# Optimization experiments

Measured on AMD Instinct MI355X. Metric: run time of the kernel, lower is better.

## Reference

```python
import jax, jax.numpy as jnp
import numpy as np

B, C_IN, N, T, E, C_OUT = 128, 32, 325, 24, 3, 64


def setup_inputs() -> dict:
    key = jax.random.key(0)
    kx, ka, kw, kb = jax.random.split(key, 4)
    x = jax.random.normal(kx, (B, C_IN, N, T), dtype=jnp.float32)
    supports = jax.random.normal(ka, (E, N, N), dtype=jnp.float32) * (1.0 / np.sqrt(N))
    # 1x1 Conv2d params: weight [c_out, c_in*(edge_dim+1)], bias [c_out]
    fan_in = C_IN * (E + 1)
    W = jax.random.normal(kw, (C_OUT, fan_in), dtype=jnp.float32) * (1.0 / np.sqrt(fan_in))
    b = jax.random.normal(kb, (C_OUT,), dtype=jnp.float32) * 0.05
    return {"x": x, "supports": supports, "W": W, "b": b}


def reference(x, supports, W, b):
    # x: [B, C, N, T], supports: [E, N, N]
    Bb, C, Nn, Tt = x.shape
    # nconv for every support at once: einsum 'bcvt,vw->bcwt' batched over E
    diff = jnp.einsum('bcvt,evw->becwt', x, supports)  # [B, E, C, N, T]
    # concat [x] + diffused copies along channel dim -> [B, (E+1)*C, N, T]
    h = jnp.concatenate([x[:, None], diff], axis=1).reshape(Bb, -1, Nn, Tt)
    # 1x1 conv == channel-mixing matmul; squeeze(-1) is a no-op since T > 1
    out = jnp.einsum('bkvt,ok->bovt', h, W) + b[None, :, None, None]
    return out  # [B, c_out, N, T]
```

## Files before the change

### kernel.cpp

```cpp
#include <hip/hip_runtime.h>
#include <hip/hip_bf16.h>

typedef short bf16x8 __attribute__((ext_vector_type(8)));
typedef short bf16x4 __attribute__((ext_vector_type(4)));
typedef float f32x4  __attribute__((ext_vector_type(4)));

static constexpr int Bb   = 128;
static constexpr int Cin  = 32;
static constexpr int Nn   = 325;
static constexpr int Tt   = 24;
static constexpr int Cout = 64;
static constexpr int NKS  = 11;
static constexpr int WP   = 336;
static constexpr int NWT  = 21;
static constexpr size_t XTB_ELEMS = (size_t)Bb * NKS * (Tt * Cin) * 32;
static constexpr size_t STP_ELEMS = (size_t)4 * NKS * WP * 32;
static constexpr size_t WB_ELEMS  = (size_t)Cout * 128;

__device__ __forceinline__ void gld16(const void* g, void* l) {
    __builtin_amdgcn_global_load_lds(
        (const __attribute__((address_space(1))) void*)g,
        (__attribute__((address_space(3))) void*)l, 16, 0, 0);
}
__device__ __forceinline__ short bfb(float f) {
    __hip_bfloat16 h = __float2bfloat16(f);
    return *reinterpret_cast<short*>(&h);
}

__global__ void build_stp(const float* __restrict__ sup,
                          __hip_bfloat16* __restrict__ stpb) {
    int idx = blockIdx.x * 256 + threadIdx.x;
    int total = 4 * NKS * WP * 32;
    if (idx >= total) return;
    int e  = idx / (NKS * WP * 32);
    int r  = idx % (NKS * WP * 32);
    int ks = r / (WP * 32);
    int r2 = r % (WP * 32);
    int w  = r2 / 32;
    int vi = r2 % 32;
    int v  = ks * 32 + vi;
    float val = 0.f;
    if (e == 0) {
        val = (v == w && v < Nn) ? 1.f : 0.f;
    } else if (v < Nn && w < Nn) {
        val = sup[((size_t)(e - 1) * Nn + v) * Nn + w];
    }
    stpb[idx] = __float2bfloat16(val);
}

__global__ void build_wb(const float* __restrict__ W,
                         __hip_bfloat16* __restrict__ Wb) {
    int i = blockIdx.x * 256 + threadIdx.x;
    if (i < Cout * 128) Wb[i] = __float2bfloat16(W[i]);
}

__global__ void transpose_x(const float* __restrict__ x,
                            __hip_bfloat16* __restrict__ xTb) {
    __shared__ __hip_bfloat16 ls[Cin * 32 * 28];
    int b  = blockIdx.x / NKS;
    int ks = blockIdx.x % NKS;
    int tid = threadIdx.x;
    for (int i = 0; i < 24; ++i) {
        int f4 = i * 256 + tid;
        int c  = f4 / 192;
        int rm = f4 % 192;
        int vi = rm / 6;
        int t0 = (rm % 6) * 4;
        int v  = ks * 32 + vi;
        float4 val = make_float4(0.f, 0.f, 0.f, 0.f);
        if (v < Nn)
            val = *(const float4*)(x + (((size_t)(b * Cin + c) * Nn + v) * Tt + t0));
        bf16x4 pk = { bfb(val.x), bfb(val.y), bfb(val.z), bfb(val.w) };
        *(bf16x4*)&ls[(c * 32 + vi) * 28 + t0] = pk;
    }
    __syncthreads();
    for (int j = 0; j < 12; ++j) {
        int o    = j * 256 + tid;
        int row  = o >> 2;
        int slot = o & 3;
        int t = row >> 5, c = row & 31;
        union { short us[8]; bf16x8 v8; } pk;
#pragma unroll
        for (int q = 0; q < 8; ++q) {
            __hip_bfloat16 h = ls[(c * 32 + slot * 8 + q) * 28 + t];
            pk.us[q] = *reinterpret_cast<short*>(&h);
        }
        *(bf16x8*)((char*)xTb + ((size_t)(b * NKS + ks) * 768 + row) * 64 + slot * 16) = pk.v8;
    }
}

__global__ __launch_bounds__(512, 2) void graphconv_main(
    const __hip_bfloat16* __restrict__ xTb,
    const __hip_bfloat16* __restrict__ stpb,
    const __hip_bfloat16* __restrict__ Wb,
    const float* __restrict__ bias,
    float* __restrict__ out) {
    __shared__ alignas(16) __hip_bfloat16 Ss[44 * 512];
    __shared__ float Os[16 * 401];

    int bid = blockIdx.x;
    int lg  = (bid & 7) * 336 + (bid >> 3);
    int b   = lg / NWT;
    int wt  = lg % NWT;
    int w0  = wt * 16;

    int tid = threadIdx.x, wid = tid >> 6, lane = tid & 63;
    int cl = lane & 15, kg = lane >> 4;

    const char* xslab = (const char*)xTb + (size_t)b * NKS * 768 * 64;
    const char* xbase = xslab + (size_t)(wid * 96 + cl) * 64 + kg * 16;

    {
        int srow  = lane >> 2;
        int sslot = ((lane & 3) ^ ((lane >> 2) & 3)) << 4;
        for (int i = wid; i < 44; i += 8) {
            int e = i / NKS, ks = i % NKS;
            gld16((const char*)stpb +
                      ((size_t)((e * NKS + ks) * WP) + w0 + srow) * 64 + sslot,
                  (char*)&Ss[0] + i * 1024 + lane * 16);
        }
    }

    bf16x8 xf[3][6];
#pragma unroll
    for (int s = 0; s < 2; ++s)
#pragma unroll
        for (int j = 0; j < 6; ++j)
            xf[s][j] = *(const bf16x8*)(xbase + (size_t)s * 49152 + (size_t)j * 1024);

    __syncthreads();

    const int asw = (kg ^ (cl & 3)) << 4;
    bf16x8 af[2][4];
#pragma unroll
    for (int e = 0; e < 4; ++e)
        af[0][e] = *(const bf16x8*)((const char*)&Ss[0] +
                                    (size_t)((e * NKS) * 16 + cl) * 64 + asw);

    f32x4 acc1[4][6] = {};
#pragma unroll
    for (int ks = 0; ks < NKS; ++ks) {
        const int cur3 = ks % 3, pf3 = (ks + 2) % 3;
        const int cur2 = ks & 1, nx2 = cur2 ^ 1;
        if (ks + 2 < NKS) {
#pragma unroll
            for (int j = 0; j < 6; ++j)
                xf[pf3][j] = *(const bf16x8*)(xbase + (size_t)(ks + 2) * 49152 +
                                              (size_t)j * 1024);
        }
        if (ks + 1 < NKS) {
#pragma unroll
            for (int e = 0; e < 4; ++e)
                af[nx2][e] = *(const bf16x8*)((const char*)&Ss[0] +
                                 (size_t)((e * NKS + ks + 1) * 16 + cl) * 64 + asw);
        }
        __builtin_amdgcn_s_setprio(1);
#pragma unroll
        for (int e = 0; e < 4; ++e)
#pragma unroll
            for (int j = 0; j < 6; ++j)
                acc1[e][j] = __builtin_amdgcn_mfma_f32_16x16x32_bf16(
                    xf[cur3][j], af[cur2][e], acc1[e][j], 0, 0, 0);
        __builtin_amdgcn_s_setprio(0);
    }

    f32x4 acc2[4][3] = {};
#pragma unroll
    for (int kappa = 0; kappa < 8; ++kappa) {
        const int e = kappa >> 1, half = kappa & 1;
        bf16x4 wf[4];
#pragma unroll
        for (int mt = 0; mt < 4; ++mt)
            wf[mt] = *(const bf16x4*)((const char*)Wb + (mt * 16 + cl) * 256 +
                                      kappa * 32 + kg * 8);
#pragma unroll
        for (int tj = 0; tj < 3; ++tj) {
            const int j = tj * 2 + half;
            f32x4 y = acc1[e][j];
            bf16x4 pb = { bfb(y[0]), bfb(y[1]), bfb(y[2]), bfb(y[3]) };
#pragma unroll
            for (int mt = 0; mt < 4; ++mt)
                acc2[mt][tj] = __builtin_amdgcn_mfma_f32_16x16x16bf16_1k(
                    wf[mt], pb, acc2[mt][tj], 0, 0, 0);
        }
    }

#pragma unroll
    for (int p = 0; p < 4; ++p) {
        if (p) __syncthreads();
#pragma unroll
        for (int tj = 0; tj < 3; ++tj) {
            const int t = wid * 3 + tj;
#pragma unroll
            for (int r = 0; r < 4; ++r)
                Os[(kg * 4 + r) * 401 + cl * 25 + t] = acc2[p][tj][r];
        }
        __syncthreads();
        const int o2 = tid >> 5, th_ = (tid >> 4) & 1, w = tid & 15;
        const int wg = w0 + w;
        if (wg < Nn) {
            const int o = p * 16 + o2;
            const float bv = bias[o];
            float f[12];
#pragma unroll
            for (int q = 0; q < 12; ++q)
                f[q] = Os[o2 * 401 + w * 25 + th_ * 12 + q] + bv;
            float* op = out + ((size_t)(b * Cout + o) * Nn + wg) * Tt + th_ * 12;
#pragma unroll
            for (int q = 0; q < 3; ++q)
                *(float4*)(op + q * 4) =
                    make_float4(f[q * 4], f[q * 4 + 1], f[q * 4 + 2], f[q * 4 + 3]);
        }
    }
}

extern "C" void kernel_launch(void* const* d_in, const int* in_sizes, int n_in,
                              void* d_out, int out_size, void* d_ws, size_t ws_size,
                              hipStream_t stream) {
    const float* x    = (const float*)d_in[0];
    const float* sup  = (const float*)d_in[1];
    const float* W    = (const float*)d_in[2];
    const float* bias = (const float*)d_in[3];
    float* out = (float*)d_out;

    __hip_bfloat16* xTb  = (__hip_bfloat16*)d_ws;
    __hip_bfloat16* stpb = xTb + XTB_ELEMS;
    __hip_bfloat16* Wb   = stpb + STP_ELEMS;

    build_stp<<<(int)((STP_ELEMS + 255) / 256), 256, 0, stream>>>(sup, stpb);
    build_wb<<<(int)((WB_ELEMS + 255) / 256), 256, 0, stream>>>(W, Wb);
    transpose_x<<<Bb * NKS, 256, 0, stream>>>(x, xTb);
    graphconv_main<<<Bb * NWT, 512, 0, stream>>>(xTb, stpb, Wb, bias, out);
}
```

Measured before the change: 315.5 us.

## Rotate k-slab start per block, remap transpose blocks to XCDs, change LDS swizzle

The main kernel now starts its reduction over the 11 node slabs at a per-block rotated offset, so concurrent blocks sharing a batch slab read different parts of it instead of all hitting the same addresses. The transpose kernel assigns batches to blocks by XCD so that each XCD's L2 holds the xTb slabs its main-kernel blocks will read. The LDS swizzle for the support tiles changes from lane bits 2-3 to bits 3-4 to cut bank conflicts. In exchange, the slab indices are runtime values, so the unrolled loop needs wraparound index arithmetic and non-constant address offsets.

```diff
diff --git a/kernel.cpp b/kernel.cpp
--- a/kernel.cpp
+++ b/kernel.cpp
@@ -57,8 +57,10 @@
 __global__ void transpose_x(const float* __restrict__ x,
                             __hip_bfloat16* __restrict__ xTb) {
     __shared__ __hip_bfloat16 ls[Cin * 32 * 28];
-    int b  = blockIdx.x / NKS;
-    int ks = blockIdx.x % NKS;
+    int xcd = blockIdx.x & 7;
+    int idx = blockIdx.x >> 3;
+    int b   = xcd * 16 + idx / NKS;
+    int ks  = idx % NKS;
     int tid = threadIdx.x;
     for (int i = 0; i < 24; ++i) {
         int f4 = i * 256 + tid;
@@ -110,9 +112,11 @@
     const char* xslab = (const char*)xTb + (size_t)b * NKS * 768 * 64;
     const char* xbase = xslab + (size_t)(wid * 96 + cl) * 64 + kg * 16;
 
+    int rot = lg % NKS;
+
     {
         int srow  = lane >> 2;
-        int sslot = ((lane & 3) ^ ((lane >> 2) & 3)) << 4;
+        int sslot = ((lane & 3) ^ ((lane >> 3) & 3)) << 4;
         for (int i = wid; i < 44; i += 8) {
             int e = i / NKS, ks = i % NKS;
             gld16((const char*)stpb +
@@ -121,38 +125,42 @@
         }
     }
 
+    int ks0 = rot;
+    int ks1 = (rot + 1 == NKS) ? 0 : rot + 1;
     bf16x8 xf[3][6];
 #pragma unroll
-    for (int s = 0; s < 2; ++s)
-#pragma unroll
-        for (int j = 0; j < 6; ++j)
-            xf[s][j] = *(const bf16x8*)(xbase + (size_t)s * 49152 + (size_t)j * 1024);
+    for (int j = 0; j < 6; ++j) {
+        xf[0][j] = *(const bf16x8*)(xbase + (size_t)ks0 * 49152 + (size_t)j * 1024);
+        xf[1][j] = *(const bf16x8*)(xbase + (size_t)ks1 * 49152 + (size_t)j * 1024);
+    }
 
     __syncthreads();
 
-    const int asw = (kg ^ (cl & 3)) << 4;
+    const int asw = (kg ^ ((cl >> 1) & 3)) << 4;
     bf16x8 af[2][4];
 #pragma unroll
     for (int e = 0; e < 4; ++e)
         af[0][e] = *(const bf16x8*)((const char*)&Ss[0] +
-                                    (size_t)((e * NKS) * 16 + cl) * 64 + asw);
+                                    (size_t)(e * NKS + ks0) * 1024 + cl * 64 + asw);
 
     f32x4 acc1[4][6] = {};
-#pragma unroll
-    for (int ks = 0; ks < NKS; ++ks) {
-        const int cur3 = ks % 3, pf3 = (ks + 2) % 3;
-        const int cur2 = ks & 1, nx2 = cur2 ^ 1;
-        if (ks + 2 < NKS) {
+    int ksp = (rot + 2 >= NKS) ? rot + 2 - NKS : rot + 2;
+    int ksn = ks1;
+#pragma unroll
+    for (int kk = 0; kk < NKS; ++kk) {
+        const int cur3 = kk % 3, pf3 = (kk + 2) % 3;
+        const int cur2 = kk & 1, nx2 = cur2 ^ 1;
+        if (kk + 2 < NKS) {
 #pragma unroll
             for (int j = 0; j < 6; ++j)
-                xf[pf3][j] = *(const bf16x8*)(xbase + (size_t)(ks + 2) * 49152 +
+                xf[pf3][j] = *(const bf16x8*)(xbase + (size_t)ksp * 49152 +
                                               (size_t)j * 1024);
         }
-        if (ks + 1 < NKS) {
+        if (kk + 1 < NKS) {
 #pragma unroll
             for (int e = 0; e < 4; ++e)
                 af[nx2][e] = *(const bf16x8*)((const char*)&Ss[0] +
-                                 (size_t)((e * NKS + ks + 1) * 16 + cl) * 64 + asw);
+                                 (size_t)(e * NKS + ksn) * 1024 + cl * 64 + asw);
         }
         __builtin_amdgcn_s_setprio(1);
 #pragma unroll
@@ -162,6 +170,8 @@
                 acc1[e][j] = __builtin_amdgcn_mfma_f32_16x16x32_bf16(
                     xf[cur3][j], af[cur2][e], acc1[e][j], 0, 0, 0);
         __builtin_amdgcn_s_setprio(0);
+        ksp = (ksp + 1 == NKS) ? 0 : ksp + 1;
+        ksn = (ksn + 1 == NKS) ? 0 : ksn + 1;
     }
 
     f32x4 acc2[4][3] = {};
```

Result: no change. 318.3 us (+0.9%).

## Split main kernel blocks by time half and remap transpose blocks per XCD

Applied to the files above, without the earlier changes.

The main graph-conv kernel now runs blocks of 256 threads, each covering half of the time axis, which doubles the grid and halves the output staging buffer. The supports tile is still loaded in full by each block, so that load is now done twice per (batch, w-tile), using a different swizzle. The transpose kernel's block index is remapped so that each XCD handles a contiguous set of batches, matching the main kernel's XCD mapping for better L2 locality. The aim is better occupancy and less LDS per block, at the cost of redundant supports loads.

```diff
diff --git a/kernel.cpp b/kernel.cpp
--- a/kernel.cpp
+++ b/kernel.cpp
@@ -13,6 +13,7 @@
 static constexpr int NKS  = 11;
 static constexpr int WP   = 336;
 static constexpr int NWT  = 21;
+static constexpr int OS1  = 210;
 static constexpr size_t XTB_ELEMS = (size_t)Bb * NKS * (Tt * Cin) * 32;
 static constexpr size_t STP_ELEMS = (size_t)4 * NKS * WP * 32;
 static constexpr size_t WB_ELEMS  = (size_t)Cout * 128;
@@ -57,8 +58,10 @@
 __global__ void transpose_x(const float* __restrict__ x,
                             __hip_bfloat16* __restrict__ xTb) {
     __shared__ __hip_bfloat16 ls[Cin * 32 * 28];
-    int b  = blockIdx.x / NKS;
-    int ks = blockIdx.x % NKS;
+    int xcd = blockIdx.x & 7;
+    int idx = blockIdx.x >> 3;
+    int b   = xcd * 16 + idx / NKS;
+    int ks  = idx % NKS;
     int tid = threadIdx.x;
     for (int i = 0; i < 24; ++i) {
         int f4 = i * 256 + tid;
@@ -89,31 +92,32 @@
     }
 }
 
-__global__ __launch_bounds__(512, 2) void graphconv_main(
+__global__ __launch_bounds__(256, 2) void graphconv_main(
     const __hip_bfloat16* __restrict__ xTb,
     const __hip_bfloat16* __restrict__ stpb,
     const __hip_bfloat16* __restrict__ Wb,
     const float* __restrict__ bias,
     float* __restrict__ out) {
     __shared__ alignas(16) __hip_bfloat16 Ss[44 * 512];
-    __shared__ float Os[16 * 401];
+    __shared__ float Os[16 * OS1];
 
     int bid = blockIdx.x;
-    int lg  = (bid & 7) * 336 + (bid >> 3);
-    int b   = lg / NWT;
-    int wt  = lg % NWT;
+    int lg  = (bid & 7) * 672 + (bid >> 3);
+    int b   = lg / 42;
+    int r   = lg % 42;
+    int wt  = r >> 1, th = r & 1;
     int w0  = wt * 16;
 
     int tid = threadIdx.x, wid = tid >> 6, lane = tid & 63;
     int cl = lane & 15, kg = lane >> 4;
 
     const char* xslab = (const char*)xTb + (size_t)b * NKS * 768 * 64;
-    const char* xbase = xslab + (size_t)(wid * 96 + cl) * 64 + kg * 16;
+    const char* xbase = xslab + (size_t)(th * 384 + wid * 96 + cl) * 64 + kg * 16;
 
     {
         int srow  = lane >> 2;
-        int sslot = ((lane & 3) ^ ((lane >> 2) & 3)) << 4;
-        for (int i = wid; i < 44; i += 8) {
+        int sslot = ((lane & 3) ^ ((lane >> 3) & 3)) << 4;
+        for (int i = wid; i < 44; i += 4) {
             int e = i / NKS, ks = i % NKS;
             gld16((const char*)stpb +
                       ((size_t)((e * NKS + ks) * WP) + w0 + srow) * 64 + sslot,
@@ -130,12 +134,12 @@
 
     __syncthreads();
 
-    const int asw = (kg ^ (cl & 3)) << 4;
+    const int asw = (kg ^ ((cl >> 1) & 3)) << 4;
     bf16x8 af[2][4];
 #pragma unroll
     for (int e = 0; e < 4; ++e)
         af[0][e] = *(const bf16x8*)((const char*)&Ss[0] +
-                                    (size_t)((e * NKS) * 16 + cl) * 64 + asw);
+                                    (size_t)(e * NKS) * 1024 + cl * 64 + asw);
 
     f32x4 acc1[4][6] = {};
 #pragma unroll
@@ -152,7 +156,7 @@
 #pragma unroll
             for (int e = 0; e < 4; ++e)
                 af[nx2][e] = *(const bf16x8*)((const char*)&Ss[0] +
-                                 (size_t)((e * NKS + ks + 1) * 16 + cl) * 64 + asw);
+                                 (size_t)(e * NKS + ks + 1) * 1024 + cl * 64 + asw);
         }
         __builtin_amdgcn_s_setprio(1);
 #pragma unroll
@@ -192,11 +196,11 @@
         for (int tj = 0; tj < 3; ++tj) {
             const int t = wid * 3 + tj;
 #pragma unroll
-            for (int r = 0; r < 4; ++r)
-                Os[(kg * 4 + r) * 401 + cl * 25 + t] = acc2[p][tj][r];
+            for (int r2_ = 0; r2_ < 4; ++r2_)
+                Os[(kg * 4 + r2_) * OS1 + cl * 13 + t] = acc2[p][tj][r2_];
         }
         __syncthreads();
-        const int o2 = tid >> 5, th_ = (tid >> 4) & 1, w = tid & 15;
+        const int o2 = tid >> 4, w = tid & 15;
         const int wg = w0 + w;
         if (wg < Nn) {
             const int o = p * 16 + o2;
@@ -204,8 +208,8 @@
             float f[12];
 #pragma unroll
             for (int q = 0; q < 12; ++q)
-                f[q] = Os[o2 * 401 + w * 25 + th_ * 12 + q] + bv;
-            float* op = out + ((size_t)(b * Cout + o) * Nn + wg) * Tt + th_ * 12;
+                f[q] = Os[o2 * OS1 + w * 13 + q] + bv;
+            float* op = out + ((size_t)(b * Cout + o) * Nn + wg) * Tt + th * 12;
 #pragma unroll
             for (int q = 0; q < 3; ++q)
                 *(float4*)(op + q * 4) =
@@ -230,5 +234,5 @@
     build_stp<<<(int)((STP_ELEMS + 255) / 256), 256, 0, stream>>>(sup, stpb);
     build_wb<<<(int)((WB_ELEMS + 255) / 256), 256, 0, stream>>>(W, Wb);
     transpose_x<<<Bb * NKS, 256, 0, stream>>>(x, xTb);
-    graphconv_main<<<Bb * NWT, 512, 0, stream>>>(xTb, stpb, Wb, bias, out);
-}
+    graphconv_main<<<Bb * NWT * 2, 256, 0, stream>>>(xTb, stpb, Wb, bias, out);
+}
```

New measurement: 309.0 us. -2.1%, faster.
